# Kernel tuning notes

Measured on AMD Instinct MI355X. Metric: run time of the kernel, lower is better.

The kernel has to match this reference:

```python
import jax, jax.numpy as jnp
import numpy as np

D = 384      # d_model
H = 6        # num_heads
K = 8        # k_neighbors
B = 8        # batch
N = 2048     # num points
EPS = 1e-5


def _layer_norm(x, g, b):
    m = jnp.mean(x, axis=-1, keepdims=True)
    v = jnp.var(x, axis=-1, keepdims=True)
    return (x - m) * jax.lax.rsqrt(v + EPS) * g + b


def setup_inputs() -> dict:
    key = jax.random.key(0)
    ks = jax.random.split(key, 12)
    s = 0.02
    return {
        "coords": jax.random.normal(ks[0], (B, 3, N), jnp.float32),
        "features": jax.random.normal(ks[1], (B, D, N), jnp.float32),
        "ln1_g": jnp.ones((D,), jnp.float32),
        "ln1_b": jnp.zeros((D,), jnp.float32),
        "w_qkv": jax.random.normal(ks[2], (D, 3 * D), jnp.float32) * s,
        "w_attn_out": jax.random.normal(ks[3], (D, D), jnp.float32) * s,
        "b_attn_out": jnp.zeros((D,), jnp.float32),
        "ga_wq": jax.random.normal(ks[4], (D, D), jnp.float32) * s,
        "ga_wk": jax.random.normal(ks[5], (D, D), jnp.float32) * s,
        "ga_wv": jax.random.normal(ks[6], (D, D), jnp.float32) * s,
        "merge_w": jax.random.normal(ks[7], (2 * D, D), jnp.float32) * s,
        "merge_b": jnp.zeros((D,), jnp.float32),
        "ln2_g": jnp.ones((D,), jnp.float32),
        "ln2_b": jnp.zeros((D,), jnp.float32),
        "ff_w1": jax.random.normal(ks[8], (D, 2 * D), jnp.float32) * s,
        "ff_b1": jnp.zeros((2 * D,), jnp.float32),
        "ff_w2": jax.random.normal(ks[9], (2 * D, D), jnp.float32) * s,
        "ff_b2": jnp.zeros((D,), jnp.float32),
    }


def reference(coords, features, ln1_g, ln1_b, w_qkv, w_attn_out, b_attn_out,
              ga_wq, ga_wk, ga_wv, merge_w, merge_b, ln2_g, ln2_b,
              ff_w1, ff_b1, ff_w2, ff_b2):
    b, d, n = features.shape
    dh = d // H
    f = jnp.swapaxes(features, 1, 2)          # [B, N, D]
    nf = _layer_norm(f, ln1_g, ln1_b)         # [B, N, D]

    # --- dense multi-head self-attention branch ---
    qkv = nf @ w_qkv                           # [B, N, 3D]
    q, k, v = jnp.split(qkv, 3, axis=-1)
    def heads(x):
        return x.reshape(b, n, H, dh).transpose(0, 2, 1, 3)  # [B, H, N, dh]
    scores = jnp.einsum('bhqd,bhkd->bhqk', heads(q), heads(k)) / jnp.sqrt(jnp.float32(dh))
    attn = jnp.einsum('bhqk,bhkd->bhqd', jax.nn.softmax(scores, axis=-1), heads(v))
    attn = attn.transpose(0, 2, 1, 3).reshape(b, n, d)
    attn = attn @ w_attn_out + b_attn_out      # output projection

    # --- KNN graph-attention branch over normalized features ---
    c = jnp.swapaxes(coords, 1, 2)             # [B, N, 3]
    sq = jnp.sum(c * c, axis=-1)               # [B, N]
    d2 = sq[:, :, None] + sq[:, None, :] - 2.0 * jnp.einsum('bnd,bmd->bnm', c, c)
    _, idx = jax.lax.top_k(-d2, K)             # [B, N, K] nearest-neighbor indices
    nbrs = jax.vmap(lambda fe, i: fe[i])(nf, idx)  # [B, N, K, D]
    gq = nf @ ga_wq                             # [B, N, D]
    gk = nbrs @ ga_wk                           # [B, N, K, D]
    gv = nbrs @ ga_wv
    gs = jnp.einsum('bnd,bnkd->bnk', gq, gk) / jnp.sqrt(jnp.float32(d))
    geom = jnp.einsum('bnk,bnkd->bnd', jax.nn.softmax(gs, axis=-1), gv)  # [B, N, D]

    # --- merge + residual + FFN ---
    merged = jnp.concatenate([attn, geom], axis=-1) @ merge_w + merge_b
    f = f + merged
    h = _layer_norm(f, ln2_g, ln2_b)
    f = f + (jax.nn.gelu(h @ ff_w1 + ff_b1) @ ff_w2 + ff_b2)
    return jnp.swapaxes(f, 1, 2)               # [B, D, N]
```

## Files before the change

kernel.cpp:

```cpp
#include <hip/hip_runtime.h>
#include <hip/hip_bf16.h>
#include <cstdint>

#define D_MODEL 384
#define NHEAD 6
#define DHEAD 64
#define NPTS 2048
#define BATCH 8

typedef __attribute__((ext_vector_type(8))) short short8;
typedef __attribute__((ext_vector_type(4))) short short4v;
typedef __attribute__((ext_vector_type(4))) float floatx4;
typedef __attribute__((ext_vector_type(2))) unsigned int u32x2;

__device__ __forceinline__ float bf2f(unsigned short u) {
    return __uint_as_float(((unsigned int)u) << 16);
}

__device__ __forceinline__ unsigned short f2bf(float f) {
    unsigned int u = __float_as_uint(f);
    unsigned int r = (u + 0x7FFFu + ((u >> 16) & 1u)) >> 16;
    return (unsigned short)r;
}

__device__ __forceinline__ unsigned cvtpk(float lo, float hi) {
    unsigned r;
    asm("v_cvt_pk_bf16_f32 %0, %1, %2" : "=v"(r) : "v"(lo), "v"(hi));
    return r;
}

__device__ __forceinline__ floatx4 mfma16(short4v a, short4v b, floatx4 c) {
#if __has_builtin(__builtin_amdgcn_mfma_f32_16x16x16bf16_1k)
    return __builtin_amdgcn_mfma_f32_16x16x16bf16_1k(a, b, c, 0, 0, 0);
#else
    floatx4 d;
    asm("v_mfma_f32_16x16x16_bf16 %0, %1, %2, %3" : "=v"(d) : "v"(a), "v"(b), "v"(c));
    return d;
#endif
}

__device__ __forceinline__ float gelu_tanh(float x) {
    float x3 = x * x * x;
    return 0.5f * x * (1.0f + tanhf(0.7978845608028654f * (x + 0.044715f * x3)));
}

__device__ __forceinline__ void gload_lds16(const unsigned short* g, unsigned short* l) {
    __builtin_amdgcn_global_load_lds(
        (const __attribute__((address_space(1))) unsigned int*)g,
        (__attribute__((address_space(3))) unsigned int*)l, 16, 0, 0);
}

__global__ __launch_bounds__(256) void k_wprep(
    const float* __restrict__ wqkv, const float* __restrict__ wao,
    const float* __restrict__ wq, const float* __restrict__ wk,
    const float* __restrict__ wv, const float* __restrict__ wm,
    const float* __restrict__ w1, const float* __restrict__ w2,
    unsigned short* __restrict__ qkvT, unsigned short* __restrict__ aoT,
    unsigned short* __restrict__ gaT, unsigned short* __restrict__ mT,
    unsigned short* __restrict__ f1T, unsigned short* __restrict__ f2T) {
    __shared__ float tile[32][33];
    int id = blockIdx.x;
    const float* src;
    unsigned short* dst;
    int K, N;
    if (id < 432)       {            src = wqkv; dst = qkvT;            K = 384; N = 1152; }
    else if (id < 576)  { id -= 432; src = wao;  dst = aoT;             K = 384; N = 384; }
    else if (id < 720)  { id -= 576; src = wq;   dst = gaT;             K = 384; N = 384; }
    else if (id < 864)  { id -= 720; src = wk;   dst = gaT + 384 * 384; K = 384; N = 384; }
    else if (id < 1008) { id -= 864; src = wv;   dst = gaT + 768 * 384; K = 384; N = 384; }
    else if (id < 1296) { id -= 1008; src = wm;  dst = mT;              K = 768; N = 384; }
    else if (id < 1584) { id -= 1296; src = w1;  dst = f1T;             K = 384; N = 768; }
    else                { id -= 1584; src = w2;  dst = f2T;             K = 768; N = 384; }
    int ntiles = N >> 5;
    int nt = id % ntiles, kt = id / ntiles;
    int tx = threadIdx.x, ty = threadIdx.y;
#pragma unroll
    for (int i = 0; i < 32; i += 8)
        tile[ty + i][tx] = src[(size_t)(kt * 32 + ty + i) * N + nt * 32 + tx];
    __syncthreads();
#pragma unroll
    for (int i = 0; i < 32; i += 8)
        dst[(size_t)(nt * 32 + ty + i) * K + kt * 32 + tx] = f2bf(tile[tx][ty + i]);
}

__global__ __launch_bounds__(256) void k_transpose_in(const float* __restrict__ feat,
                                                      unsigned short* __restrict__ f) {
    __shared__ float tile[32][33];
    int b = blockIdx.z;
    int n0 = blockIdx.x * 32, d0 = blockIdx.y * 32;
    int tx = threadIdx.x, ty = threadIdx.y;
#pragma unroll
    for (int i = 0; i < 32; i += 8)
        tile[ty + i][tx] = feat[((size_t)b * D_MODEL + d0 + ty + i) * NPTS + n0 + tx];
    __syncthreads();
#pragma unroll
    for (int i = 0; i < 32; i += 8)
        f[((size_t)b * NPTS + n0 + ty + i) * D_MODEL + d0 + tx] = f2bf(tile[tx][ty + i]);
}

__global__ __launch_bounds__(256) void k_transpose_out(const unsigned short* __restrict__ f,
                                                       float* __restrict__ out) {
    __shared__ float tile[32][33];
    int b = blockIdx.z;
    int d0 = blockIdx.x * 32, n0 = blockIdx.y * 32;
    int tx = threadIdx.x, ty = threadIdx.y;
#pragma unroll
    for (int i = 0; i < 32; i += 8)
        tile[ty + i][tx] = bf2f(f[((size_t)b * NPTS + n0 + ty + i) * D_MODEL + d0 + tx]);
    __syncthreads();
#pragma unroll
    for (int i = 0; i < 32; i += 8)
        out[((size_t)b * D_MODEL + d0 + ty + i) * NPTS + n0 + tx] = tile[tx][ty + i];
}

__global__ __launch_bounds__(256) void k_vt(const unsigned short* __restrict__ qkv,
                                            unsigned short* __restrict__ vt) {
    __shared__ unsigned short tile[32][33];
    int b = blockIdx.z;
    int h = blockIdx.y >> 1, d0 = (blockIdx.y & 1) * 32;
    int n0 = blockIdx.x * 32;
    int tx = threadIdx.x, ty = threadIdx.y;
#pragma unroll
    for (int i = 0; i < 32; i += 8)
        tile[ty + i][tx] =
            qkv[((size_t)b * NPTS + n0 + ty + i) * 1152 + 768 + h * 64 + d0 + tx];
    __syncthreads();
#pragma unroll
    for (int i = 0; i < 32; i += 8)
        vt[(((size_t)(b * NHEAD + h) * 64) + d0 + ty + i) * NPTS + n0 + tx] = tile[tx][ty + i];
}

__global__ __launch_bounds__(128) void k_layernorm(const unsigned short* __restrict__ x,
                                                   const float* __restrict__ g,
                                                   const float* __restrict__ bt,
                                                   unsigned short* __restrict__ y) {
    int row = blockIdx.x, t = threadIdx.x;
    const unsigned short* xr = x + (size_t)row * D_MODEL;
    float v0 = bf2f(xr[t]), v1 = bf2f(xr[t + 128]), v2 = bf2f(xr[t + 256]);
    float s = v0 + v1 + v2;
    float s2 = v0 * v0 + v1 * v1 + v2 * v2;
#pragma unroll
    for (int off = 32; off > 0; off >>= 1) {
        s += __shfl_xor(s, off, 64);
        s2 += __shfl_xor(s2, off, 64);
    }
    __shared__ float ps[2], ps2[2];
    if ((t & 63) == 0) { ps[t >> 6] = s; ps2[t >> 6] = s2; }
    __syncthreads();
    s = ps[0] + ps[1];
    s2 = ps2[0] + ps2[1];
    float mean = s * (1.0f / 384.0f);
    float var = s2 * (1.0f / 384.0f) - mean * mean;
    var = fmaxf(var, 0.0f);
    float inv = 1.0f / sqrtf(var + 1e-5f);
    unsigned short* yr = y + (size_t)row * D_MODEL;
    yr[t]       = f2bf((v0 - mean) * inv * g[t]       + bt[t]);
    yr[t + 128] = f2bf((v1 - mean) * inv * g[t + 128] + bt[t + 128]);
    yr[t + 256] = f2bf((v2 - mean) * inv * g[t + 256] + bt[t + 256]);
}

__global__ __launch_bounds__(256) void k_knn(const float* __restrict__ coords,
                                             int* __restrict__ idx) {
    __shared__ float4 cpts[NPTS];
    int b = blockIdx.x >> 9;
    int q0 = (blockIdx.x & 511) * 4;
    const float* cb = coords + (size_t)b * 3 * NPTS;
    int tid = threadIdx.x;
#pragma unroll
    for (int i = 0; i < 8; i++) {
        int m = tid + i * 256;
        float x = cb[m], y = cb[NPTS + m], z = cb[2 * NPTS + m];
        float sq = __fadd_rn(__fadd_rn(__fmul_rn(x, x), __fmul_rn(y, y)), __fmul_rn(z, z));
        cpts[m] = make_float4(x, y, z, sq);
    }
    __syncthreads();
    int wv = tid >> 6, lane = tid & 63;
    int n = q0 + wv;
    float4 qp = cpts[n];
    float qx = qp.x, qy = qp.y, qz = qp.z, sqn = qp.w;
    unsigned keys[32];
    unsigned h[8];
#pragma unroll
    for (int k = 0; k < 8; k++) h[k] = 0xFFFFFFFFu;
#pragma unroll
    for (int j = 0; j < 32; j++) {
        float4 cp = cpts[j * 64 + lane];
        float dot = __fadd_rn(__fadd_rn(__fmul_rn(qx, cp.x), __fmul_rn(qy, cp.y)),
                              __fmul_rn(qz, cp.z));
        float d2 = __fsub_rn(__fadd_rn(sqn, cp.w), __fmul_rn(2.0f, dot));
        unsigned u = __float_as_uint(d2);
        u ^= (unsigned)(((int)u >> 31)) | 0x80000000u;
        keys[j] = u;
        unsigned cur = u;
#pragma unroll
        for (int t2 = 0; t2 < 8; t2++) {
            unsigned lo = h[t2] < cur ? h[t2] : cur;
            cur = h[t2] < cur ? cur : h[t2];
            h[t2] = lo;
        }
    }
    unsigned curh = h[0];
    unsigned T8 = 0;
#pragma unroll
    for (int r = 0; r < 8; r++) {
        unsigned w = curh;
#pragma unroll
        for (int off = 1; off < 64; off <<= 1) {
            unsigned o = __shfl_xor(w, off, 64);
            w = o < w ? o : w;
        }
        T8 = w;
        if (r < 7) {
            unsigned long long mask = __ballot(curh == w);
            if (curh == w && (mask & ((1ull << lane) - 1ull)) == 0) {
#pragma unroll
                for (int t2 = 0; t2 < 7; t2++) h[t2] = h[t2 + 1];
                h[7] = 0xFFFFFFFFu;
                curh = h[0];
            }
        }
    }
    int* outr = idx + ((size_t)b * NPTS + n) * 8;
    int cnt = 0;
    unsigned meq = 0xFFFFFFFFu;
#pragma unroll
    for (int j = 0; j < 32; j++) {
        unsigned m = (unsigned)(j * 64 + lane);
        bool strict = keys[j] < T8;
        unsigned long long msk = __ballot(strict);
        if (strict) {
            int pos = cnt + (int)__popcll(msk & ((1ull << lane) - 1ull));
            outr[pos] = (int)m;
        }
        cnt += (int)__popcll(msk);
        if (keys[j] == T8 && m < meq) meq = m;
    }
    while (cnt < 8) {
        unsigned w = meq;
#pragma unroll
        for (int off = 1; off < 64; off <<= 1) {
            unsigned o = __shfl_xor(w, off, 64);
            w = o < w ? o : w;
        }
        bool winner = (meq == w);
        if (winner) outr[cnt] = (int)w;
        cnt++;
        if (cnt >= 8) break;
        if (winner) {
            meq = 0xFFFFFFFFu;
#pragma unroll
            for (int j = 0; j < 32; j++) {
                unsigned m = (unsigned)(j * 64 + lane);
                if (keys[j] == T8 && m > w && m < meq) meq = m;
            }
        }
    }
}

__global__ __launch_bounds__(256) void k_gemm(const unsigned short* __restrict__ A, int lda,
                                              const unsigned short* __restrict__ WT,
                                              const float* __restrict__ bias,
                                              const unsigned short* __restrict__ res,
                                              unsigned short* __restrict__ C, int ldc,
                                              int K, int act, int NX) {
    __shared__ unsigned short Alds[2 * 128 * 32];
    __shared__ unsigned short Wlds[2 * 128 * 32];
    int tid = threadIdx.x;
    int wv = tid >> 6, lane = tid & 63;
    int l15 = lane & 15, quad = lane >> 4;
    int id = blockIdx.x;
    int xcd = id & 7, slot = id >> 3;
    int y = xcd * 16 + slot / NX;
    int x = slot % NX;
    int row0 = y * 128, col0 = x * 128;
    int wm = wv >> 1, wn = wv & 1;
    int wbase = tid & 192;
    floatx4 acc[4][4];
#pragma unroll
    for (int i = 0; i < 4; i++)
#pragma unroll
        for (int j = 0; j < 4; j++) acc[i][j] = (floatx4){0.f, 0.f, 0.f, 0.f};
    for (int k0 = 0; k0 < K; k0 += 64) {
#pragma unroll
        for (int i = 0; i < 4; i++) {
            int idx = i * 256 + tid;
            int kc = idx >> 9, row = (idx >> 2) & 127, ko = idx & 3;
            unsigned short* ldst = Alds + (size_t)(i * 256 + wbase) * 8;
            gload_lds16(A + (size_t)(row0 + row) * lda + k0 + kc * 32 + ko * 8, ldst);
            unsigned short* ldstw = Wlds + (size_t)(i * 256 + wbase) * 8;
            gload_lds16(WT + (size_t)(col0 + row) * K + k0 + kc * 32 + ko * 8, ldstw);
        }
        __syncthreads();
#pragma unroll
        for (int kc = 0; kc < 2; kc++) {
            short8 af[4], bf[4];
#pragma unroll
            for (int i = 0; i < 4; i++)
                af[i] = *(const short8*)&Alds[kc * 4096 + (wm * 64 + i * 16 + l15) * 32 + quad * 8];
#pragma unroll
            for (int j = 0; j < 4; j++)
                bf[j] = *(const short8*)&Wlds[kc * 4096 + (wn * 64 + j * 16 + l15) * 32 + quad * 8];
#pragma unroll
            for (int i = 0; i < 4; i++)
#pragma unroll
                for (int j = 0; j < 4; j++)
                    acc[i][j] =
                        __builtin_amdgcn_mfma_f32_16x16x32_bf16(bf[j], af[i], acc[i][j], 0, 0, 0);
        }
        __syncthreads();
    }
#pragma unroll
    for (int i = 0; i < 4; i++) {
        int r = row0 + wm * 64 + i * 16 + l15;
#pragma unroll
        for (int j = 0; j < 4; j++) {
            int cb = col0 + wn * 64 + j * 16 + quad * 4;
            float4 bv = bias ? *(const float4*)(bias + cb) : make_float4(0.f, 0.f, 0.f, 0.f);
            float v0 = acc[i][j][0] + bv.x;
            float v1 = acc[i][j][1] + bv.y;
            float v2 = acc[i][j][2] + bv.z;
            float v3 = acc[i][j][3] + bv.w;
            if (act == 1) {
                v0 = gelu_tanh(v0); v1 = gelu_tanh(v1);
                v2 = gelu_tanh(v2); v3 = gelu_tanh(v3);
            }
            if (res) {
                uint2 rv = *(const uint2*)(res + (size_t)r * ldc + cb);
                const unsigned short* rs = (const unsigned short*)&rv;
                v0 += bf2f(rs[0]); v1 += bf2f(rs[1]);
                v2 += bf2f(rs[2]); v3 += bf2f(rs[3]);
            }
            ushort4 u;
            u.x = f2bf(v0); u.y = f2bf(v1); u.z = f2bf(v2); u.w = f2bf(v3);
            *(ushort4*)(C + (size_t)r * ldc + cb) = u;
        }
    }
}

__global__ __launch_bounds__(256, 3) void k_attn(const unsigned short* __restrict__ qkv,
                                                 const unsigned short* __restrict__ vt,
                                                 unsigned short* __restrict__ attn) {
    __shared__ unsigned short Klds[2][64 * 64];
    __shared__ unsigned short VTl[4][64 * 64];
    int id = blockIdx.x;
    int xcd = id & 7, slot = id >> 3;
    int pair = xcd * 6 + (slot >> 4);
    int tile = slot & 15;
    int b = pair / 6, h = pair % 6;
    int tid = threadIdx.x;
    int wv = tid >> 6, lane = tid & 63;
    int l15 = lane & 15, quad = lane >> 4;
    int qbase = tile * 128 + wv * 32;
    const unsigned short* qkvb = qkv + (size_t)b * NPTS * 1152;
    const unsigned short* vtb = vt + (size_t)(b * NHEAD + h) * 64 * NPTS;
    const float SC = 0.18033688011112042f;
    short8 qf[2][2];
#pragma unroll
    for (int qt = 0; qt < 2; qt++) {
        const unsigned short* qptr =
            qkvb + (size_t)(qbase + qt * 16 + l15) * 1152 + h * 64 + quad * 8;
        qf[qt][0] = *(const short8*)qptr;
        qf[qt][1] = *(const short8*)(qptr + 32);
#pragma unroll
        for (int g = 0; g < 2; g++) {
            short8 v = qf[qt][g];
#pragma unroll
            for (int e = 0; e < 8; e++)
                v[e] = (short)f2bf(bf2f((unsigned short)v[e]) * SC);
            qf[qt][g] = v;
        }
    }
    short4v ones4;
#pragma unroll
    for (int e = 0; e < 4; e++) ones4[e] = (short)0x3F80;
    int x7 = l15 & 7;
    int sk0 = ((quad ^ x7) << 4);
    int sk1 = (((quad + 4) ^ x7) << 4);
    int vslot[4];
#pragma unroll
    for (int kt = 0; kt < 4; kt++) vslot[kt] = (((kt * 2 + (quad >> 1)) ^ x7) << 4);
    int vsub = (quad & 1) * 8;
    int sdg = tid & 7;
    floatx4 o[2][4];
#pragma unroll
    for (int qt = 0; qt < 2; qt++)
#pragma unroll
        for (int ct = 0; ct < 4; ct++) o[qt][ct] = (floatx4){0.f, 0.f, 0.f, 0.f};
    floatx4 l4[2];
    l4[0] = (floatx4){0.f, 0.f, 0.f, 0.f};
    l4[1] = (floatx4){0.f, 0.f, 0.f, 0.f};

    auto stage = [&](int t) {
        int k0 = t * 64;
#pragma unroll
        for (int i = 0; i < 2; i++) {
            int sid = i * 256 + tid;
            int row = sid >> 3;
            int sl = sdg ^ (row & 7);
            gload_lds16(qkvb + (size_t)(k0 + row) * 1152 + 384 + h * 64 + sl * 8,
                        &Klds[t & 1][(size_t)(i * 256 + (tid & 192)) * 8]);
            gload_lds16(vtb + (size_t)row * NPTS + k0 + sl * 8,
                        &VTl[t & 3][(size_t)(i * 256 + (tid & 192)) * 8]);
        }
    };
    auto qkchain = [&](int t, short4v (&pfc)[2][4]) {
        const char* Kb = (const char*)&Klds[t & 1][0];
        short8 kf[4][2];
#pragma unroll
        for (int ct = 0; ct < 4; ct++) {
            kf[ct][0] = *(const short8*)(Kb + (ct * 16 + l15) * 128 + sk0);
            kf[ct][1] = *(const short8*)(Kb + (ct * 16 + l15) * 128 + sk1);
        }
#pragma unroll
        for (int qt = 0; qt < 2; qt++) {
#pragma unroll
            for (int ct = 0; ct < 4; ct++) {
                floatx4 z = (floatx4){0.f, 0.f, 0.f, 0.f};
                z = __builtin_amdgcn_mfma_f32_16x16x32_bf16(kf[ct][0], qf[qt][0], z, 0, 0, 0);
                z = __builtin_amdgcn_mfma_f32_16x16x32_bf16(kf[ct][1], qf[qt][1], z, 0, 0, 0);
                float p0 = __builtin_amdgcn_exp2f(z[0]);
                float p1 = __builtin_amdgcn_exp2f(z[1]);
                float p2 = __builtin_amdgcn_exp2f(z[2]);
                float p3 = __builtin_amdgcn_exp2f(z[3]);
                u32x2 pk;
                pk.x = cvtpk(p0, p1);
                pk.y = cvtpk(p2, p3);
                pfc[qt][ct] = __builtin_bit_cast(short4v, pk);
            }
        }
    };
    auto pv = [&](int t, short4v (&pfp)[2][4]) {
        const char* Vb = (const char*)&VTl[t & 3][0] + l15 * 128 + vsub;
#pragma unroll
        for (int ctd = 0; ctd < 4; ctd++) {
            short4v va[4];
#pragma unroll
            for (int kt = 0; kt < 4; kt++)
                va[kt] = *(const short4v*)(Vb + ctd * 2048 + vslot[kt]);
#pragma unroll
            for (int kt = 0; kt < 4; kt++)
#pragma unroll
                for (int qt = 0; qt < 2; qt++)
                    o[qt][ctd] = mfma16(va[kt], pfp[qt][kt], o[qt][ctd]);
        }
#pragma unroll
        for (int qt = 0; qt < 2; qt++)
#pragma unroll
            for (int kt = 0; kt < 4; kt++) l4[qt] = mfma16(ones4, pfp[qt][kt], l4[qt]);
    };

    short4v pfA[2][4], pfB[2][4];
    stage(0);
    __syncthreads();
    stage(1);
    qkchain(0, pfA);
    __syncthreads();
    for (int tt = 0; tt < 15; ++tt) {
        int t1 = 2 * tt + 1, t2 = 2 * tt + 2;
        stage(t1 + 1);
        qkchain(t1, pfB);
        pv(t1 - 1, pfA);
        __syncthreads();
        stage(t2 + 1);
        qkchain(t2, pfA);
        pv(t2 - 1, pfB);
        __syncthreads();
    }
    qkchain(31, pfB);
    pv(30, pfA);
    pv(31, pfB);

#pragma unroll
    for (int qt = 0; qt < 2; qt++) {
        float linv = 1.0f / l4[qt][0];
#pragma unroll
        for (int ct = 0; ct < 4; ct++) {
            ushort4 u;
            u.x = f2bf(o[qt][ct][0] * linv);
            u.y = f2bf(o[qt][ct][1] * linv);
            u.z = f2bf(o[qt][ct][2] * linv);
            u.w = f2bf(o[qt][ct][3] * linv);
            *(ushort4*)(attn + ((size_t)b * NPTS + qbase + qt * 16 + l15) * 384 + h * 64 +
                        ct * 16 + quad * 4) = u;
        }
    }
}

__global__ __launch_bounds__(64) void k_geom(const unsigned short* __restrict__ gap,
                                             const int* __restrict__ idx,
                                             unsigned short* __restrict__ cat) {
    int r = blockIdx.x;
    int b = r >> 11;
    int t = threadIdx.x;
    int nb[8];
#pragma unroll
    for (int k = 0; k < 8; k++) nb[k] = idx[(size_t)r * 8 + k];
    const unsigned short* gqr = gap + (size_t)r * 1152;
    float qv[6];
#pragma unroll
    for (int j = 0; j < 6; j++) qv[j] = bf2f(gqr[t + 64 * j]);
    float s[8];
#pragma unroll
    for (int k = 0; k < 8; k++) {
        const unsigned short* nkr = gap + ((size_t)b * NPTS + nb[k]) * 1152 + 384;
        float acc = 0.0f;
#pragma unroll
        for (int j = 0; j < 6; j++) acc += qv[j] * bf2f(nkr[t + 64 * j]);
#pragma unroll
        for (int mm = 32; mm > 0; mm >>= 1) acc += __shfl_xor(acc, mm, 64);
        s[k] = acc * 0.05103103630798287f;
    }
    float mx = s[0];
#pragma unroll
    for (int k = 1; k < 8; k++) mx = fmaxf(mx, s[k]);
    float w[8];
    float sum = 0.0f;
#pragma unroll
    for (int k = 0; k < 8; k++) { w[k] = __expf(s[k] - mx); sum += w[k]; }
    float inv = 1.0f / sum;
    unsigned short* outr = cat + (size_t)r * 768 + 384;
#pragma unroll
    for (int j = 0; j < 6; j++) {
        int d = t + 64 * j;
        float acc = 0.0f;
#pragma unroll
        for (int k = 0; k < 8; k++)
            acc += w[k] * bf2f(gap[((size_t)b * NPTS + nb[k]) * 1152 + 768 + d]);
        outr[d] = f2bf(acc * inv);
    }
}

extern "C" void kernel_launch(void* const* d_in, const int* in_sizes, int n_in,
                              void* d_out, int out_size, void* d_ws, size_t ws_size,
                              hipStream_t stream) {
    (void)in_sizes; (void)n_in; (void)out_size; (void)ws_size;
    const float* coords     = (const float*)d_in[0];
    const float* features   = (const float*)d_in[1];
    const float* ln1_g      = (const float*)d_in[2];
    const float* ln1_b      = (const float*)d_in[3];
    const float* w_qkv      = (const float*)d_in[4];
    const float* w_attn_out = (const float*)d_in[5];
    const float* b_attn_out = (const float*)d_in[6];
    const float* ga_wq      = (const float*)d_in[7];
    const float* ga_wk      = (const float*)d_in[8];
    const float* ga_wv      = (const float*)d_in[9];
    const float* merge_w    = (const float*)d_in[10];
    const float* merge_b    = (const float*)d_in[11];
    const float* ln2_g      = (const float*)d_in[12];
    const float* ln2_b      = (const float*)d_in[13];
    const float* ff_w1      = (const float*)d_in[14];
    const float* ff_b1      = (const float*)d_in[15];
    const float* ff_w2      = (const float*)d_in[16];
    const float* ff_b2      = (const float*)d_in[17];

    unsigned short* W0 = (unsigned short*)d_ws;
    const size_t SZ = (size_t)BATCH * NPTS * D_MODEL;
    unsigned short* F    = W0 + 0 * SZ;
    unsigned short* NF   = W0 + 1 * SZ;
    unsigned short* QKV  = W0 + 2 * SZ;
    unsigned short* ATTN = W0 + 5 * SZ;
    unsigned short* VT   = W0 + 6 * SZ;
    unsigned short* CAT  = W0 + 2 * SZ;
    unsigned short* GAP  = W0 + 4 * SZ;
    unsigned short* F2   = W0 + 4 * SZ;
    unsigned short* HB   = W0 + 1 * SZ;
    unsigned short* T1   = W0 + 5 * SZ;
    unsigned short* FFIN = W0 + 2 * SZ;
    int*            IDX  = (int*)(W0 + 7 * SZ);
    unsigned short* WTS  = W0 + 7 * SZ + 262144;
    unsigned short* qkvT = WTS;
    unsigned short* aoT  = qkvT + 442368;
    unsigned short* gaT  = aoT + 147456;
    unsigned short* mT   = gaT + 442368;
    unsigned short* f1T  = mT + 294912;
    unsigned short* f2T  = f1T + 294912;

    const int M = BATCH * NPTS;

    k_wprep<<<1872, dim3(32, 8), 0, stream>>>(w_qkv, w_attn_out, ga_wq, ga_wk, ga_wv,
                                              merge_w, ff_w1, ff_w2,
                                              qkvT, aoT, gaT, mT, f1T, f2T);
    k_transpose_in<<<dim3(NPTS / 32, D_MODEL / 32, BATCH), dim3(32, 8), 0, stream>>>(features, F);
    k_layernorm<<<M, 128, 0, stream>>>(F, ln1_g, ln1_b, NF);
    k_knn<<<BATCH * (NPTS / 4), 256, 0, stream>>>(coords, IDX);
    k_gemm<<<9 * 128, 256, 0, stream>>>(NF, 384, qkvT, nullptr, nullptr,
                                        QKV, 1152, 384, 0, 9);
    k_vt<<<dim3(NPTS / 32, 2 * NHEAD, BATCH), dim3(32, 8), 0, stream>>>(QKV, VT);
    k_attn<<<768, 256, 0, stream>>>(QKV, VT, ATTN);
    k_gemm<<<3 * 128, 256, 0, stream>>>(ATTN, 384, aoT, b_attn_out, nullptr,
                                        CAT, 768, 384, 0, 3);
    k_gemm<<<9 * 128, 256, 0, stream>>>(NF, 384, gaT, nullptr, nullptr,
                                        GAP, 1152, 384, 0, 9);
    k_geom<<<M, 64, 0, stream>>>(GAP, IDX, CAT);
    k_gemm<<<3 * 128, 256, 0, stream>>>(CAT, 768, mT, merge_b, F,
                                        F2, 384, 768, 0, 3);
    k_layernorm<<<M, 128, 0, stream>>>(F2, ln2_g, ln2_b, HB);
    k_gemm<<<6 * 128, 256, 0, stream>>>(HB, 384, f1T, ff_b1, nullptr,
                                        T1, 768, 384, 1, 6);
    k_gemm<<<3 * 128, 256, 0, stream>>>(T1, 768, f2T, ff_b2, F2,
                                        FFIN, 384, 768, 0, 3);
    k_transpose_out<<<dim3(D_MODEL / 32, NPTS / 32, BATCH), dim3(32, 8), 0, stream>>>(
        FFIN, (float*)d_out);
}
```

Measured before the change: 431.2 us.

## Double-buffer LDS tiles in GEMM to overlap global loads with MFMA

Converts the k_gemm main loop from a single LDS buffer loaded 64 K-elements at a time into a two-buffer pipeline of 32-element K stages. The next stage's global-to-LDS loads are issued before the MFMAs on the current buffer, so load latency can hide behind compute. Each K step now needs one barrier instead of two. The trade-off is more, smaller iterations, and correctness relies on the barrier also waiting for the async LDS loads to finish.

```diff
diff --git a/kernel.cpp b/kernel.cpp
--- a/kernel.cpp
+++ b/kernel.cpp
@@ -263,8 +263,8 @@
                                               const unsigned short* __restrict__ res,
                                               unsigned short* __restrict__ C, int ldc,
                                               int K, int act, int NX) {
-    __shared__ unsigned short Alds[2 * 128 * 32];
-    __shared__ unsigned short Wlds[2 * 128 * 32];
+    __shared__ unsigned short Alds[2][128 * 32];
+    __shared__ unsigned short Wlds[2][128 * 32];
     int tid = threadIdx.x;
     int wv = tid >> 6, lane = tid & 63;
     int l15 = lane & 15, quad = lane >> 4;
@@ -280,34 +280,37 @@
     for (int i = 0; i < 4; i++)
 #pragma unroll
         for (int j = 0; j < 4; j++) acc[i][j] = (floatx4){0.f, 0.f, 0.f, 0.f};
-    for (int k0 = 0; k0 < K; k0 += 64) {
-#pragma unroll
-        for (int i = 0; i < 4; i++) {
-            int idx = i * 256 + tid;
-            int kc = idx >> 9, row = (idx >> 2) & 127, ko = idx & 3;
-            unsigned short* ldst = Alds + (size_t)(i * 256 + wbase) * 8;
-            gload_lds16(A + (size_t)(row0 + row) * lda + k0 + kc * 32 + ko * 8, ldst);
-            unsigned short* ldstw = Wlds + (size_t)(i * 256 + wbase) * 8;
-            gload_lds16(WT + (size_t)(col0 + row) * K + k0 + kc * 32 + ko * 8, ldstw);
-        }
-        __syncthreads();
-#pragma unroll
-        for (int kc = 0; kc < 2; kc++) {
-            short8 af[4], bf[4];
-#pragma unroll
-            for (int i = 0; i < 4; i++)
-                af[i] = *(const short8*)&Alds[kc * 4096 + (wm * 64 + i * 16 + l15) * 32 + quad * 8];
+    auto stage = [&](int bu, int k0) {
+#pragma unroll
+        for (int i = 0; i < 2; i++) {
+            int sid = i * 256 + tid;
+            int row = sid >> 2, ko = sid & 3;
+            gload_lds16(A + (size_t)(row0 + row) * lda + k0 + ko * 8,
+                        &Alds[bu][(size_t)(i * 256 + wbase) * 8]);
+            gload_lds16(WT + (size_t)(col0 + row) * K + k0 + ko * 8,
+                        &Wlds[bu][(size_t)(i * 256 + wbase) * 8]);
+        }
+    };
+    int nst = K >> 5;
+    stage(0, 0);
+    __syncthreads();
+    for (int t = 0; t < nst; ++t) {
+        int bu = t & 1;
+        if (t + 1 < nst) stage(bu ^ 1, (t + 1) * 32);
+        short8 af[4], bf[4];
+#pragma unroll
+        for (int i = 0; i < 4; i++)
+            af[i] = *(const short8*)&Alds[bu][(wm * 64 + i * 16 + l15) * 32 + quad * 8];
+#pragma unroll
+        for (int j = 0; j < 4; j++)
+            bf[j] = *(const short8*)&Wlds[bu][(wn * 64 + j * 16 + l15) * 32 + quad * 8];
+#pragma unroll
+        for (int i = 0; i < 4; i++)
 #pragma unroll
             for (int j = 0; j < 4; j++)
-                bf[j] = *(const short8*)&Wlds[kc * 4096 + (wn * 64 + j * 16 + l15) * 32 + quad * 8];
-#pragma unroll
-            for (int i = 0; i < 4; i++)
-#pragma unroll
-                for (int j = 0; j < 4; j++)
-                    acc[i][j] =
-                        __builtin_amdgcn_mfma_f32_16x16x32_bf16(bf[j], af[i], acc[i][j], 0, 0, 0);
-        }
-        __syncthreads();
+                acc[i][j] =
+                    __builtin_amdgcn_mfma_f32_16x16x32_bf16(bf[j], af[i], acc[i][j], 0, 0, 0);
+        if (t + 1 < nst) __syncthreads();
     }
 #pragma unroll
     for (int i = 0; i < 4; i++) {
```

Result: faster. 422.5 us (-2.0%).
